# Performance work log

Measured on AMD Instinct MI355X. Metric: run time of the kernel, lower is better.

## Reference

```python
import jax, jax.numpy as jnp
import numpy as np

B, L, DX, H = 2, 2048, 1024, 16
DQ = DK = DV = DR = 64


def setup_inputs() -> dict:
    key0 = jax.random.key(0)
    ks = jax.random.split(key0, 14)
    def lin(kw, kb, din, dout):
        s = 1.0 / np.sqrt(din)
        w = jax.random.uniform(kw, (din, dout), jnp.float32, -s, s)
        b = jax.random.uniform(kb, (dout,), jnp.float32, -s, s)
        return w, b
    value = jax.random.normal(ks[0], (B, L, DX), jnp.float32)
    key_t = jax.random.normal(ks[1], (B, L, DX), jnp.float32)
    query = jax.random.normal(ks[2], (B, L, DX), jnp.float32)
    mask = jnp.tril(jnp.ones((L, L), jnp.int32))[None, None]  # [1,1,L,L] causal
    Wq_w, Wq_b = lin(ks[3], ks[4], DX, DQ * H)
    Wk_w, Wk_b = lin(ks[5], ks[6], DX, DK * H)
    Wv_w, Wv_b = lin(ks[7], ks[8], DX, DV * H)
    Wr_w, Wr_b = lin(ks[9], ks[10], DX, DR * H)
    wo_w, wo_b = lin(ks[11], ks[12], DV * H, DX)
    return dict(value=value, key=key_t, query=query, mask=mask,
                Wq_w=Wq_w, Wq_b=Wq_b, Wk_w=Wk_w, Wk_b=Wk_b,
                Wv_w=Wv_w, Wv_b=Wv_b, Wr_w=Wr_w, Wr_b=Wr_b,
                wo_w=wo_w, wo_b=wo_b)


def reference(value, key, query, mask, Wq_w, Wq_b, Wk_w, Wk_b, Wv_w, Wv_b,
              Wr_w, Wr_b, wo_w, wo_b):
    N, Lq, _ = query.shape
    q = (query @ Wq_w + Wq_b).reshape(N, Lq, H, DQ)   # nqhd
    k = (key @ Wk_w + Wk_b).reshape(N, -1, H, DK)     # nkhd
    v = (value @ Wv_w + Wv_b).reshape(N, -1, H, DV)   # nlhd
    r = (query @ Wr_w + Wr_b).reshape(N, Lq, H, DR)   # computed but unused (as in source)
    del r
    scores = jnp.einsum('nqhd,nkhd->nhqk', q, k)      # [N,H,L,L] materialized
    scores = jnp.where(mask == 0, jnp.float32(-1e20), scores)
    scale = jnp.float32(np.sqrt(DX))  # source divides by embedding_size**0.5
    attn = jax.nn.softmax(scores / scale, axis=3)
    out = jnp.einsum('nhql,nlhd->nqhd', attn, v).reshape(N, Lq, H * DV)
    return out @ wo_w + wo_b
```

## Files before the change

### kernel.cpp

```cpp
#include <hip/hip_runtime.h>
#include <hip/hip_bf16.h>
#include <type_traits>

typedef __hip_bfloat16 bf16;
typedef __attribute__((ext_vector_type(4))) float f32x4;
typedef __attribute__((ext_vector_type(8))) short s16x8;

#define DEVINL __device__ __forceinline__

#if defined(__has_builtin) && __has_builtin(__builtin_amdgcn_exp2f)
#define FEXP2(x) __builtin_amdgcn_exp2f(x)
#else
#define FEXP2(x) __exp2f(x)
#endif

DEVINL s16x8 load16B(const void* p) {
  s16x8 v;
  __builtin_memcpy(&v, __builtin_assume_aligned(p, 16), 16);
  return v;
}
DEVINL void store16B(void* p, s16x8 v) {
  __builtin_memcpy(__builtin_assume_aligned(p, 16), &v, 16);
}
DEVINL s16x8 cvt8(const float* p) {
  f32x4 a, b;
  __builtin_memcpy(&a, __builtin_assume_aligned(p, 16), 16);
  __builtin_memcpy(&b, __builtin_assume_aligned(p + 4, 16), 16);
  union { s16x8 v; bf16 h[8]; } u;
#pragma unroll
  for (int i = 0; i < 4; i++) {
    u.h[i] = __float2bfloat16(a[i]);
    u.h[4 + i] = __float2bfloat16(b[i]);
  }
  return u.v;
}
DEVINL void gload_lds16(const bf16* g, bf16* l) {
  __builtin_amdgcn_global_load_lds(
      (__attribute__((address_space(1))) void*)(void*)const_cast<bf16*>(g),
      (__attribute__((address_space(3))) void*)l, 16, 0, 0);
}

static constexpr int SEQ = 2048;
#define QSCALE 0.04508422002778011f

__global__ __launch_bounds__(256) void k_transpose(
    const float* __restrict__ Wq, const float* __restrict__ Wk,
    const float* __restrict__ Wv, const float* __restrict__ Wo,
    bf16* __restrict__ dst) {
  __shared__ float t[64][65];
  const float* src = blockIdx.z == 0 ? Wq : blockIdx.z == 1 ? Wk
                   : blockIdx.z == 2 ? Wv : Wo;
  bf16* out = dst + (size_t)blockIdx.z * 1024 * 1024;
  const int r0 = blockIdx.y * 64, c0 = blockIdx.x * 64;
#pragma unroll
  for (int i = 0; i < 16; i++) {
    int e = i * 256 + threadIdx.x;
    int r = e >> 6, c = e & 63;
    t[r][c] = src[(size_t)(r0 + r) * 1024 + c0 + c];
  }
  __syncthreads();
#pragma unroll
  for (int i = 0; i < 16; i++) {
    int e = i * 256 + threadIdx.x;
    int r = e >> 6, c = e & 63;
    out[(size_t)(c0 + r) * 1024 + r0 + c] = __float2bfloat16(t[c][r]);
  }
}

__global__ __launch_bounds__(256) void k_cvt3(
    const float* __restrict__ q, const float* __restrict__ k,
    const float* __restrict__ v, bf16* __restrict__ dstbase) {
  const float* src = blockIdx.z == 0 ? q : blockIdx.z == 1 ? k : v;
  bf16* dst = dstbase + (size_t)blockIdx.z * 4194304;
  size_t i = ((size_t)blockIdx.x * 256 + threadIdx.x) * 8;
  store16B(dst + i, cvt8(src + i));
}

template <typename XT, int MODE>
DEVINL void gemm_body(const XT* __restrict__ X, const bf16* __restrict__ WT,
                      const float* __restrict__ bias, void* __restrict__ dstv,
                      const float scale, const int m0, const int n0,
                      bf16* As, bf16* Bs) {
  const int tid = threadIdx.x;
  const int w = tid >> 6, lane = tid & 63, lg = lane >> 4, li = lane & 15;
  const int wm = w >> 1, wn = w & 1;

  f32x4 acc[4][4] = {};

  for (int kt = 0; kt < 32; ++kt) {
    const int k0 = kt * 32;
#pragma unroll
    for (int j = 0; j < 2; j++) {
      const int cb = (j * 4 + w) * 64;
      const int c = cb + lane;
      const int r = c >> 2, kk = (c & 3) * 8;
      gload_lds16(WT + (size_t)(n0 + r) * 1024 + k0 + kk, Bs + cb * 8);
      if constexpr (std::is_same_v<XT, bf16>)
        gload_lds16(X + (size_t)(m0 + r) * 1024 + k0 + kk, As + cb * 8);
    }
    if constexpr (std::is_same_v<XT, float>) {
#pragma unroll
      for (int j = 0; j < 2; j++) {
        const int c = j * 256 + tid;
        const int r = c >> 2, kk = (c & 3) * 8;
        s16x8 a = cvt8(X + (size_t)(m0 + r) * 1024 + k0 + kk);
        store16B((char*)As + c * 16, a);
      }
    }
    __syncthreads();
    s16x8 af[4], bfv[4];
#pragma unroll
    for (int i = 0; i < 4; i++)
      af[i] = load16B((char*)As + (wm * 64 + i * 16 + li) * 64 + lg * 16);
#pragma unroll
    for (int j = 0; j < 4; j++)
      bfv[j] = load16B((char*)Bs + (wn * 64 + j * 16 + li) * 64 + lg * 16);
#pragma unroll
    for (int i = 0; i < 4; i++)
#pragma unroll
      for (int j = 0; j < 4; j++) {
        if constexpr (MODE == 0)
          acc[i][j] = __builtin_amdgcn_mfma_f32_16x16x32_bf16(
              bfv[j], af[i], acc[i][j], 0, 0, 0);
        else
          acc[i][j] = __builtin_amdgcn_mfma_f32_16x16x32_bf16(
              af[i], bfv[j], acc[i][j], 0, 0, 0);
      }
    __syncthreads();
  }

  if constexpr (MODE == 1) {
    bf16* dst = (bf16*)dstv;
#pragma unroll
    for (int j = 0; j < 4; j++) {
      const int n = n0 + wn * 64 + j * 16 + li;
      const float bv = bias[n];
#pragma unroll
      for (int i = 0; i < 4; i++) {
        const int mrow = m0 + wm * 64 + i * 16 + lg * 4;
        f32x4 a = acc[i][j];
        size_t base =
            (((size_t)(mrow >> 11) * 16 + (n >> 6)) * 64 + (n & 63)) * SEQ +
            (mrow & 2047);
        bf16 tmp[4];
#pragma unroll
        for (int r = 0; r < 4; r++) tmp[r] = __float2bfloat16(a[r] + bv);
        __builtin_memcpy(__builtin_assume_aligned(dst + base, 8), tmp, 8);
      }
    }
  } else if constexpr (MODE == 2) {
    float* dst = (float*)dstv;
#pragma unroll
    for (int j = 0; j < 4; j++) {
      const int n = n0 + wn * 64 + j * 16 + li;
      const float bv = bias[n];
#pragma unroll
      for (int i = 0; i < 4; i++) {
        const int mrow = m0 + wm * 64 + i * 16 + lg * 4;
        f32x4 a = acc[i][j];
#pragma unroll
        for (int r = 0; r < 4; r++)
          dst[(size_t)(mrow + r) * 1024 + n] = a[r] + bv;
      }
    }
  } else {
    f32x4 bias4[4];
#pragma unroll
    for (int j = 0; j < 4; j++)
      __builtin_memcpy(&bias4[j], bias + n0 + wn * 64 + j * 16 + lg * 4, 16);
    bf16* dst = (bf16*)dstv;
#pragma unroll
    for (int i = 0; i < 4; i++) {
      const int m = m0 + wm * 64 + i * 16 + li;
      const int l = m & 2047, bb = m >> 11;
#pragma unroll
      for (int j = 0; j < 4; j++) {
        const int nb = n0 + wn * 64 + j * 16 + lg * 4;
        bf16 tmp[4];
#pragma unroll
        for (int r = 0; r < 4; r++)
          tmp[r] = __float2bfloat16((acc[i][j][r] + bias4[j][r]) * scale);
        size_t idx = (((size_t)bb * 16 + (nb >> 6)) * SEQ + l) * 64 + (nb & 63);
        __builtin_memcpy(__builtin_assume_aligned(dst + idx, 8), tmp, 8);
      }
    }
  }
}

__global__ __launch_bounds__(256) void k_gemm_qkv_bf16(
    const bf16* __restrict__ xbase, const bf16* __restrict__ WTbase,
    const float* __restrict__ qb, const float* __restrict__ kb,
    const float* __restrict__ vb, bf16* __restrict__ qo,
    bf16* __restrict__ ko, bf16* __restrict__ vto) {
  __shared__ alignas(16) bf16 As[128 * 32];
  __shared__ alignas(16) bf16 Bs[128 * 32];
  const int z = blockIdx.z;
  const bf16* X = xbase + (size_t)z * 4194304;
  const bf16* WT = WTbase + (size_t)z * 1048576;
  const float* bias = z == 0 ? qb : z == 1 ? kb : vb;
  if (z == 2)
    gemm_body<bf16, 1>(X, WT, bias, (void*)vto, 1.0f, blockIdx.x * 128,
                       blockIdx.y * 128, As, Bs);
  else
    gemm_body<bf16, 0>(X, WT, bias, z == 0 ? (void*)qo : (void*)ko,
                       z == 0 ? QSCALE : 1.0f, blockIdx.x * 128,
                       blockIdx.y * 128, As, Bs);
}

__global__ __launch_bounds__(256) void k_gemm_qkv_f32(
    const float* __restrict__ qx, const float* __restrict__ kx,
    const float* __restrict__ vx, const bf16* __restrict__ WTbase,
    const float* __restrict__ qb, const float* __restrict__ kb,
    const float* __restrict__ vb, bf16* __restrict__ qo,
    bf16* __restrict__ ko, bf16* __restrict__ vto) {
  __shared__ alignas(16) bf16 As[128 * 32];
  __shared__ alignas(16) bf16 Bs[128 * 32];
  const int z = blockIdx.z;
  const float* X = z == 0 ? qx : z == 1 ? kx : vx;
  const bf16* WT = WTbase + (size_t)z * 1048576;
  const float* bias = z == 0 ? qb : z == 1 ? kb : vb;
  if (z == 2)
    gemm_body<float, 1>(X, WT, bias, (void*)vto, 1.0f, blockIdx.x * 128,
                        blockIdx.y * 128, As, Bs);
  else
    gemm_body<float, 0>(X, WT, bias, z == 0 ? (void*)qo : (void*)ko,
                        z == 0 ? QSCALE : 1.0f, blockIdx.x * 128,
                        blockIdx.y * 128, As, Bs);
}

__global__ __launch_bounds__(256) void k_gemm_out(
    const bf16* __restrict__ X, const bf16* __restrict__ WT,
    const float* __restrict__ bias, float* __restrict__ out) {
  __shared__ alignas(16) bf16 As[128 * 32];
  __shared__ alignas(16) bf16 Bs[128 * 32];
  gemm_body<bf16, 2>(X, WT, bias, (void*)out, 1.0f, blockIdx.x * 128,
                     blockIdx.y * 128, As, Bs);
}

__global__ __launch_bounds__(256) void k_attn(
    const bf16* __restrict__ qb, const bf16* __restrict__ kb,
    const bf16* __restrict__ vtb, bf16* __restrict__ attn) {
  __shared__ alignas(16) bf16 Ks[2][64 * 64];
  __shared__ alignas(16) bf16 Vts[2][64 * 64];
  __shared__ alignas(16) bf16 Ps[4][16 * 64];
  const int tid = threadIdx.x;
  const int w = tid >> 6, lane = tid & 63, lg = lane >> 4, li = lane & 15;
  const int bh = blockIdx.x;
  const int y = blockIdx.y;
  const bf16* qh = qb + (size_t)bh * SEQ * 64;
  const bf16* kh = kb + (size_t)bh * SEQ * 64;
  const bf16* vth = vtb + (size_t)bh * 64 * SEQ;

  const int c0s = tid, c1s = 256 + tid;
  const int by0 = (c0s * 16) ^ (((c0s >> 3) & 7) << 4);
  const int by1 = (c1s * 16) ^ (((c1s >> 3) & 7) << 4);
  const int d0 = c0s >> 3, kk0 = (c0s & 7) * 8;
  const int d1 = c1s >> 3, kk1 = (c1s & 7) * 8;
  const int psw = (li & 7) << 3;
  const int b = bh >> 4, h = bh & 15;
  const int sb = (lane & 48);

#pragma unroll
  for (int half = 0; half < 2; half++) {
    const int qblk = half == 0 ? 31 - y : y;
    const int qrow = qblk * 64 + w * 16;

    s16x8 aq[2];
#pragma unroll
    for (int c = 0; c < 2; c++)
      aq[c] = load16B(qh + (size_t)(qrow + li) * 64 + c * 32 + lg * 8);

    f32x4 o[4] = {};
    float m_run = -1e38f;
    float l_run = 0.f;

    s16x8 rk[2], rv[2];
    rk[0] = load16B(kh + (size_t)c0s * 8);
    rk[1] = load16B(kh + (size_t)c1s * 8);
    rv[0] = load16B(vth + (size_t)d0 * SEQ + kk0);
    rv[1] = load16B(vth + (size_t)d1 * SEQ + kk1);
    store16B((char*)Ks[0] + by0, rk[0]);
    store16B((char*)Ks[0] + by1, rk[1]);
    store16B((char*)Vts[0] + by0, rv[0]);
    store16B((char*)Vts[0] + by1, rv[1]);
    if (qblk >= 1) {
      rk[0] = load16B(kh + (size_t)64 * 64 + c0s * 8);
      rk[1] = load16B(kh + (size_t)64 * 64 + c1s * 8);
      rv[0] = load16B(vth + (size_t)d0 * SEQ + 64 + kk0);
      rv[1] = load16B(vth + (size_t)d1 * SEQ + 64 + kk1);
    }
    __syncthreads();

    for (int kbk = 0; kbk <= qblk; ++kbk) {
      const int cur = kbk & 1;
      if (kbk < qblk) {
        store16B((char*)Ks[cur ^ 1] + by0, rk[0]);
        store16B((char*)Ks[cur ^ 1] + by1, rk[1]);
        store16B((char*)Vts[cur ^ 1] + by0, rv[0]);
        store16B((char*)Vts[cur ^ 1] + by1, rv[1]);
        if (kbk + 2 <= qblk) {
          const int kn = (kbk + 2) * 64;
          rk[0] = load16B(kh + (size_t)kn * 64 + c0s * 8);
          rk[1] = load16B(kh + (size_t)kn * 64 + c1s * 8);
          rv[0] = load16B(vth + (size_t)d0 * SEQ + kn + kk0);
          rv[1] = load16B(vth + (size_t)d1 * SEQ + kn + kk1);
        }
      }

      f32x4 s[4];
      __builtin_amdgcn_s_setprio(1);
#pragma unroll
      for (int t = 0; t < 4; t++) {
        f32x4 z = {};
#pragma unroll
        for (int c = 0; c < 2; c++) {
          int row = t * 16 + li;
          s16x8 ak =
              load16B((char*)Ks[cur] +
                      ((row * 128 + c * 64 + lg * 16) ^ ((row & 7) << 4)));
          z = __builtin_amdgcn_mfma_f32_16x16x32_bf16(ak, aq[c], z, 0, 0, 0);
        }
        s[t] = z;
      }
      __builtin_amdgcn_s_setprio(0);

      if (kbk == qblk) {
        const int kb0 = kbk * 64 + lg * 4;
        const int qg = qrow + li;
#pragma unroll
        for (int t = 0; t < 4; t++)
#pragma unroll
          for (int r = 0; r < 4; r++)
            if (kb0 + t * 16 + r > qg) s[t][r] = -1e30f;
      }

      f32x4 mm = s[0];
#pragma unroll
      for (int t = 1; t < 4; t++)
#pragma unroll
        for (int r = 0; r < 4; r++) mm[r] = fmaxf(mm[r], s[t][r]);
      float mr = fmaxf(fmaxf(mm[0], mm[1]), fmaxf(mm[2], mm[3]));
      mr = fmaxf(mr, __shfl_xor(mr, 16));
      mr = fmaxf(mr, __shfl_xor(mr, 32));

      const bool grow = !__all(mr <= m_run + 8.0f);
      const float mn = grow ? fmaxf(m_run, mr) : m_run;

      float p[4][4];
      float s0 = 0.f, s1 = 0.f, s2 = 0.f, s3 = 0.f;
#pragma unroll
      for (int r = 0; r < 4; r++) {
        float p0 = FEXP2(s[0][r] - mn), p1 = FEXP2(s[1][r] - mn);
        float p2 = FEXP2(s[2][r] - mn), p3 = FEXP2(s[3][r] - mn);
        p[0][r] = p0; p[1][r] = p1; p[2][r] = p2; p[3][r] = p3;
        s0 += p0; s1 += p1; s2 += p2; s3 += p3;
      }
      float sum = (s0 + s1) + (s2 + s3);
      sum += __shfl_xor(sum, 16);
      sum += __shfl_xor(sum, 32);

      if (grow) {
        const float cr = FEXP2(m_run - mn);
        l_run = l_run * cr + sum;
        m_run = mn;
        float crr[4];
#pragma unroll
        for (int r = 0; r < 4; r++) crr[r] = __shfl(cr, sb + (sb >> 2) + r);
#pragma unroll
        for (int t = 0; t < 4; t++)
#pragma unroll
          for (int r = 0; r < 4; r++) o[t][r] *= crr[r];
      } else {
        l_run += sum;
      }

#pragma unroll
      for (int t = 0; t < 4; t++) {
        bf16 tmp[4];
#pragma unroll
        for (int r = 0; r < 4; r++) tmp[r] = __float2bfloat16(p[t][r]);
        __builtin_memcpy(
            __builtin_assume_aligned(
                &Ps[w][li * 64 + ((t * 16 + lg * 4) ^ psw)], 8),
            tmp, 8);
      }

      s16x8 ap[2];
#pragma unroll
      for (int c = 0; c < 2; c++)
        ap[c] = load16B(&Ps[w][li * 64 + ((c * 32 + lg * 8) ^ psw)]);

      __builtin_amdgcn_s_setprio(1);
#pragma unroll
      for (int t = 0; t < 4; t++) {
#pragma unroll
        for (int c = 0; c < 2; c++) {
          int row = t * 16 + li;
          s16x8 bv =
              load16B((char*)Vts[cur] +
                      ((row * 128 + c * 64 + lg * 16) ^ ((row & 7) << 4)));
          o[t] =
              __builtin_amdgcn_mfma_f32_16x16x32_bf16(ap[c], bv, o[t], 0, 0, 0);
        }
      }
      __builtin_amdgcn_s_setprio(0);
      __syncthreads();
    }

    const float inv = 1.0f / l_run;
    float invr[4];
#pragma unroll
    for (int r = 0; r < 4; r++) invr[r] = __shfl(inv, sb + (sb >> 2) + r);
#pragma unroll
    for (int r = 0; r < 4; r++)
#pragma unroll
      for (int t = 0; t < 4; t++) {
        size_t idx = (size_t)(b * SEQ + qrow + lg * 4 + r) * 1024 + h * 64 +
                     t * 16 + li;
        attn[idx] = __float2bfloat16(o[t][r] * invr[r]);
      }
  }
}

extern "C" void kernel_launch(void* const* d_in, const int* in_sizes, int n_in,
                              void* d_out, int out_size, void* d_ws,
                              size_t ws_size, hipStream_t stream) {
  (void)in_sizes; (void)n_in; (void)out_size;
  const float* value = (const float*)d_in[0];
  const float* key   = (const float*)d_in[1];
  const float* query = (const float*)d_in[2];
  const float* Wq_w = (const float*)d_in[4];
  const float* Wq_b = (const float*)d_in[5];
  const float* Wk_w = (const float*)d_in[6];
  const float* Wk_b = (const float*)d_in[7];
  const float* Wv_w = (const float*)d_in[8];
  const float* Wv_b = (const float*)d_in[9];
  const float* wo_w = (const float*)d_in[12];
  const float* wo_b = (const float*)d_in[13];

  bf16* ws = (bf16*)d_ws;
  const size_t MM = 1048576;
  bf16* WT = ws;

  k_transpose<<<dim3(16, 16, 4), 256, 0, stream>>>(Wq_w, Wk_w, Wv_w, wo_w, WT);

  if (ws_size >= 28ull * MM * 2) {
    bf16* xbuf = ws + 4 * MM;
    bf16* qbuf = ws + 16 * MM;
    bf16* kbuf = ws + 20 * MM;
    bf16* vtbf = ws + 24 * MM;
    bf16* abuf = ws + 4 * MM;
    k_cvt3<<<dim3(2048, 1, 3), 256, 0, stream>>>(query, key, value, xbuf);
    k_gemm_qkv_bf16<<<dim3(32, 8, 3), 256, 0, stream>>>(
        xbuf, WT, Wq_b, Wk_b, Wv_b, qbuf, kbuf, vtbf);
    k_attn<<<dim3(32, 16), 256, 0, stream>>>(qbuf, kbuf, vtbf, abuf);
    k_gemm_out<<<dim3(32, 8), 256, 0, stream>>>(abuf, WT + 3 * MM, wo_b,
                                                (float*)d_out);
  } else {
    bf16* qbuf = ws + 4 * MM;
    bf16* kbuf = ws + 8 * MM;
    bf16* vtbf = ws + 12 * MM;
    bf16* abuf = ws + 16 * MM;
    k_gemm_qkv_f32<<<dim3(32, 8, 3), 256, 0, stream>>>(
        query, key, value, WT, Wq_b, Wk_b, Wv_b, qbuf, kbuf, vtbf);
    k_attn<<<dim3(32, 16), 256, 0, stream>>>(qbuf, kbuf, vtbf, abuf);
    k_gemm_out<<<dim3(32, 8), 256, 0, stream>>>(abuf, WT + 3 * MM, wo_b,
                                                (float*)d_out);
  }
}
```

Before: 126.7 us.

## Split long causal attention query blocks over KV halves and merge partials

Each attention block now handles one query block instead of a paired long/short pair. The 16 longest query blocks per head are split into two KV-range halves, each writing unnormalized bf16 partial outputs plus running max and sum. A new combine kernel merges the halves with the log-sum-exp rescale. This is meant to balance work across more blocks (1536 instead of 512) and shorten the critical path, at the cost of an extra launch, partial-output traffic, and bf16 rounding of the partials.

```diff
diff --git a/kernel.cpp b/kernel.cpp
--- a/kernel.cpp
+++ b/kernel.cpp
@@ -237,9 +237,11 @@
                      blockIdx.y * 128, As, Bs);
 }
 
+template <bool SPLIT>
 __global__ __launch_bounds__(256) void k_attn(
     const bf16* __restrict__ qb, const bf16* __restrict__ kb,
-    const bf16* __restrict__ vtb, bf16* __restrict__ attn) {
+    const bf16* __restrict__ vtb, bf16* __restrict__ attn,
+    bf16* __restrict__ po_base, float* __restrict__ pml_base) {
   __shared__ alignas(16) bf16 Ks[2][64 * 64];
   __shared__ alignas(16) bf16 Vts[2][64 * 64];
   __shared__ alignas(16) bf16 Ps[4][16 * 64];
@@ -247,9 +249,35 @@
   const int w = tid >> 6, lane = tid & 63, lg = lane >> 4, li = lane & 15;
   const int bh = blockIdx.x;
   const int y = blockIdx.y;
+  int qblk, kstart, kend, pidx;
+  if constexpr (SPLIT) {
+    if (y < 32) {
+      qblk = 31 - (y >> 1);
+      const int part = y & 1;
+      const int half = (qblk + 1) >> 1;
+      kstart = part ? half : 0;
+      kend = part ? qblk : half - 1;
+      pidx = ((bh << 4) + (qblk - 16)) * 2 + part;
+    } else {
+      qblk = 47 - y; kstart = 0; kend = qblk; pidx = -1;
+    }
+  } else {
+    qblk = (y < 8) ? 31 - y : (y < 16) ? y + 8 : (y < 24) ? 31 - y : y - 24;
+    kstart = 0; kend = qblk; pidx = -1;
+  }
+  const int qrow = qblk * 64 + w * 16;
   const bf16* qh = qb + (size_t)bh * SEQ * 64;
   const bf16* kh = kb + (size_t)bh * SEQ * 64;
   const bf16* vth = vtb + (size_t)bh * 64 * SEQ;
+
+  s16x8 aq[2];
+#pragma unroll
+  for (int c = 0; c < 2; c++)
+    aq[c] = load16B(qh + (size_t)(qrow + li) * 64 + c * 32 + lg * 8);
+
+  f32x4 o[4] = {};
+  float m_run = -1e38f;
+  float l_run = 0.f;
 
   const int c0s = tid, c1s = 256 + tid;
   const int by0 = (c0s * 16) ^ (((c0s >> 3) & 7) << 4);
@@ -257,156 +285,161 @@
   const int d0 = c0s >> 3, kk0 = (c0s & 7) * 8;
   const int d1 = c1s >> 3, kk1 = (c1s & 7) * 8;
   const int psw = (li & 7) << 3;
-  const int b = bh >> 4, h = bh & 15;
   const int sb = (lane & 48);
 
-#pragma unroll
-  for (int half = 0; half < 2; half++) {
-    const int qblk = half == 0 ? 31 - y : y;
-    const int qrow = qblk * 64 + w * 16;
-
-    s16x8 aq[2];
-#pragma unroll
-    for (int c = 0; c < 2; c++)
-      aq[c] = load16B(qh + (size_t)(qrow + li) * 64 + c * 32 + lg * 8);
-
-    f32x4 o[4] = {};
-    float m_run = -1e38f;
-    float l_run = 0.f;
-
-    s16x8 rk[2], rv[2];
-    rk[0] = load16B(kh + (size_t)c0s * 8);
-    rk[1] = load16B(kh + (size_t)c1s * 8);
-    rv[0] = load16B(vth + (size_t)d0 * SEQ + kk0);
-    rv[1] = load16B(vth + (size_t)d1 * SEQ + kk1);
+  s16x8 rk[2], rv[2];
+  {
+    const int k0b = kstart * 64;
+    rk[0] = load16B(kh + (size_t)k0b * 64 + c0s * 8);
+    rk[1] = load16B(kh + (size_t)k0b * 64 + c1s * 8);
+    rv[0] = load16B(vth + (size_t)d0 * SEQ + k0b + kk0);
+    rv[1] = load16B(vth + (size_t)d1 * SEQ + k0b + kk1);
     store16B((char*)Ks[0] + by0, rk[0]);
     store16B((char*)Ks[0] + by1, rk[1]);
     store16B((char*)Vts[0] + by0, rv[0]);
     store16B((char*)Vts[0] + by1, rv[1]);
-    if (qblk >= 1) {
-      rk[0] = load16B(kh + (size_t)64 * 64 + c0s * 8);
-      rk[1] = load16B(kh + (size_t)64 * 64 + c1s * 8);
-      rv[0] = load16B(vth + (size_t)d0 * SEQ + 64 + kk0);
-      rv[1] = load16B(vth + (size_t)d1 * SEQ + 64 + kk1);
-    }
+    if (kstart + 1 <= kend) {
+      const int k1b = (kstart + 1) * 64;
+      rk[0] = load16B(kh + (size_t)k1b * 64 + c0s * 8);
+      rk[1] = load16B(kh + (size_t)k1b * 64 + c1s * 8);
+      rv[0] = load16B(vth + (size_t)d0 * SEQ + k1b + kk0);
+      rv[1] = load16B(vth + (size_t)d1 * SEQ + k1b + kk1);
+    }
+  }
+  __syncthreads();
+
+  for (int kbk = kstart; kbk <= kend; ++kbk) {
+    const int cur = (kbk - kstart) & 1;
+    if (kbk < kend) {
+      store16B((char*)Ks[cur ^ 1] + by0, rk[0]);
+      store16B((char*)Ks[cur ^ 1] + by1, rk[1]);
+      store16B((char*)Vts[cur ^ 1] + by0, rv[0]);
+      store16B((char*)Vts[cur ^ 1] + by1, rv[1]);
+      if (kbk + 2 <= kend) {
+        const int kn = (kbk + 2) * 64;
+        rk[0] = load16B(kh + (size_t)kn * 64 + c0s * 8);
+        rk[1] = load16B(kh + (size_t)kn * 64 + c1s * 8);
+        rv[0] = load16B(vth + (size_t)d0 * SEQ + kn + kk0);
+        rv[1] = load16B(vth + (size_t)d1 * SEQ + kn + kk1);
+      }
+    }
+
+    f32x4 s[4];
+    __builtin_amdgcn_s_setprio(1);
+#pragma unroll
+    for (int t = 0; t < 4; t++) {
+      f32x4 z = {};
+#pragma unroll
+      for (int c = 0; c < 2; c++) {
+        int row = t * 16 + li;
+        s16x8 ak = load16B((char*)Ks[cur] +
+                           ((row * 128 + c * 64 + lg * 16) ^ ((row & 7) << 4)));
+        z = __builtin_amdgcn_mfma_f32_16x16x32_bf16(ak, aq[c], z, 0, 0, 0);
+      }
+      s[t] = z;
+    }
+    __builtin_amdgcn_s_setprio(0);
+
+    if (kbk == qblk) {
+      const int kb0 = kbk * 64 + lg * 4;
+      const int qg = qrow + li;
+#pragma unroll
+      for (int t = 0; t < 4; t++)
+#pragma unroll
+        for (int r = 0; r < 4; r++)
+          if (kb0 + t * 16 + r > qg) s[t][r] = -1e30f;
+    }
+
+    f32x4 mm = s[0];
+#pragma unroll
+    for (int t = 1; t < 4; t++)
+#pragma unroll
+      for (int r = 0; r < 4; r++) mm[r] = fmaxf(mm[r], s[t][r]);
+    float mr = fmaxf(fmaxf(mm[0], mm[1]), fmaxf(mm[2], mm[3]));
+    mr = fmaxf(mr, __shfl_xor(mr, 16));
+    mr = fmaxf(mr, __shfl_xor(mr, 32));
+
+    const bool grow = !__all(mr <= m_run + 8.0f);
+    const float mn = grow ? fmaxf(m_run, mr) : m_run;
+
+    float p[4][4];
+    float s0 = 0.f, s1 = 0.f, s2 = 0.f, s3 = 0.f;
+#pragma unroll
+    for (int r = 0; r < 4; r++) {
+      float p0 = FEXP2(s[0][r] - mn), p1 = FEXP2(s[1][r] - mn);
+      float p2 = FEXP2(s[2][r] - mn), p3 = FEXP2(s[3][r] - mn);
+      p[0][r] = p0; p[1][r] = p1; p[2][r] = p2; p[3][r] = p3;
+      s0 += p0; s1 += p1; s2 += p2; s3 += p3;
+    }
+    float sum = (s0 + s1) + (s2 + s3);
+    sum += __shfl_xor(sum, 16);
+    sum += __shfl_xor(sum, 32);
+
+    if (grow) {
+      const float cr = FEXP2(m_run - mn);
+      l_run = l_run * cr + sum;
+      m_run = mn;
+      float crr[4];
+#pragma unroll
+      for (int r = 0; r < 4; r++) crr[r] = __shfl(cr, sb + (sb >> 2) + r);
+#pragma unroll
+      for (int t = 0; t < 4; t++)
+#pragma unroll
+        for (int r = 0; r < 4; r++) o[t][r] *= crr[r];
+    } else {
+      l_run += sum;
+    }
+
+#pragma unroll
+    for (int t = 0; t < 4; t++) {
+      bf16 tmp[4];
+#pragma unroll
+      for (int r = 0; r < 4; r++) tmp[r] = __float2bfloat16(p[t][r]);
+      __builtin_memcpy(
+          __builtin_assume_aligned(
+              &Ps[w][li * 64 + ((t * 16 + lg * 4) ^ psw)], 8),
+          tmp, 8);
+    }
+
+    s16x8 ap[2];
+#pragma unroll
+    for (int c = 0; c < 2; c++)
+      ap[c] = load16B(&Ps[w][li * 64 + ((c * 32 + lg * 8) ^ psw)]);
+
+    __builtin_amdgcn_s_setprio(1);
+#pragma unroll
+    for (int t = 0; t < 4; t++) {
+#pragma unroll
+      for (int c = 0; c < 2; c++) {
+        int row = t * 16 + li;
+        s16x8 bv = load16B((char*)Vts[cur] +
+                           ((row * 128 + c * 64 + lg * 16) ^ ((row & 7) << 4)));
+        o[t] = __builtin_amdgcn_mfma_f32_16x16x32_bf16(ap[c], bv, o[t], 0, 0, 0);
+      }
+    }
+    __builtin_amdgcn_s_setprio(0);
     __syncthreads();
-
-    for (int kbk = 0; kbk <= qblk; ++kbk) {
-      const int cur = kbk & 1;
-      if (kbk < qblk) {
-        store16B((char*)Ks[cur ^ 1] + by0, rk[0]);
-        store16B((char*)Ks[cur ^ 1] + by1, rk[1]);
-        store16B((char*)Vts[cur ^ 1] + by0, rv[0]);
-        store16B((char*)Vts[cur ^ 1] + by1, rv[1]);
-        if (kbk + 2 <= qblk) {
-          const int kn = (kbk + 2) * 64;
-          rk[0] = load16B(kh + (size_t)kn * 64 + c0s * 8);
-          rk[1] = load16B(kh + (size_t)kn * 64 + c1s * 8);
-          rv[0] = load16B(vth + (size_t)d0 * SEQ + kn + kk0);
-          rv[1] = load16B(vth + (size_t)d1 * SEQ + kn + kk1);
-        }
-      }
-
-      f32x4 s[4];
-      __builtin_amdgcn_s_setprio(1);
-#pragma unroll
-      for (int t = 0; t < 4; t++) {
-        f32x4 z = {};
-#pragma unroll
-        for (int c = 0; c < 2; c++) {
-          int row = t * 16 + li;
-          s16x8 ak =
-              load16B((char*)Ks[cur] +
-                      ((row * 128 + c * 64 + lg * 16) ^ ((row & 7) << 4)));
-          z = __builtin_amdgcn_mfma_f32_16x16x32_bf16(ak, aq[c], z, 0, 0, 0);
-        }
-        s[t] = z;
-      }
-      __builtin_amdgcn_s_setprio(0);
-
-      if (kbk == qblk) {
-        const int kb0 = kbk * 64 + lg * 4;
-        const int qg = qrow + li;
-#pragma unroll
-        for (int t = 0; t < 4; t++)
-#pragma unroll
-          for (int r = 0; r < 4; r++)
-            if (kb0 + t * 16 + r > qg) s[t][r] = -1e30f;
-      }
-
-      f32x4 mm = s[0];
-#pragma unroll
-      for (int t = 1; t < 4; t++)
-#pragma unroll
-        for (int r = 0; r < 4; r++) mm[r] = fmaxf(mm[r], s[t][r]);
-      float mr = fmaxf(fmaxf(mm[0], mm[1]), fmaxf(mm[2], mm[3]));
-      mr = fmaxf(mr, __shfl_xor(mr, 16));
-      mr = fmaxf(mr, __shfl_xor(mr, 32));
-
-      const bool grow = !__all(mr <= m_run + 8.0f);
-      const float mn = grow ? fmaxf(m_run, mr) : m_run;
-
-      float p[4][4];
-      float s0 = 0.f, s1 = 0.f, s2 = 0.f, s3 = 0.f;
-#pragma unroll
-      for (int r = 0; r < 4; r++) {
-        float p0 = FEXP2(s[0][r] - mn), p1 = FEXP2(s[1][r] - mn);
-        float p2 = FEXP2(s[2][r] - mn), p3 = FEXP2(s[3][r] - mn);
-        p[0][r] = p0; p[1][r] = p1; p[2][r] = p2; p[3][r] = p3;
-        s0 += p0; s1 += p1; s2 += p2; s3 += p3;
-      }
-      float sum = (s0 + s1) + (s2 + s3);
-      sum += __shfl_xor(sum, 16);
-      sum += __shfl_xor(sum, 32);
-
-      if (grow) {
-        const float cr = FEXP2(m_run - mn);
-        l_run = l_run * cr + sum;
-        m_run = mn;
-        float crr[4];
-#pragma unroll
-        for (int r = 0; r < 4; r++) crr[r] = __shfl(cr, sb + (sb >> 2) + r);
-#pragma unroll
-        for (int t = 0; t < 4; t++)
-#pragma unroll
-          for (int r = 0; r < 4; r++) o[t][r] *= crr[r];
-      } else {
-        l_run += sum;
-      }
-
-#pragma unroll
-      for (int t = 0; t < 4; t++) {
-        bf16 tmp[4];
-#pragma unroll
-        for (int r = 0; r < 4; r++) tmp[r] = __float2bfloat16(p[t][r]);
-        __builtin_memcpy(
-            __builtin_assume_aligned(
-                &Ps[w][li * 64 + ((t * 16 + lg * 4) ^ psw)], 8),
-            tmp, 8);
-      }
-
-      s16x8 ap[2];
-#pragma unroll
-      for (int c = 0; c < 2; c++)
-        ap[c] = load16B(&Ps[w][li * 64 + ((c * 32 + lg * 8) ^ psw)]);
-
-      __builtin_amdgcn_s_setprio(1);
-#pragma unroll
-      for (int t = 0; t < 4; t++) {
-#pragma unroll
-        for (int c = 0; c < 2; c++) {
-          int row = t * 16 + li;
-          s16x8 bv =
-              load16B((char*)Vts[cur] +
-                      ((row * 128 + c * 64 + lg * 16) ^ ((row & 7) << 4)));
-          o[t] =
-              __builtin_amdgcn_mfma_f32_16x16x32_bf16(ap[c], bv, o[t], 0, 0, 0);
-        }
-      }
-      __builtin_amdgcn_s_setprio(0);
-      __syncthreads();
-    }
-
+  }
+
+  if (SPLIT && pidx >= 0) {
+    bf16* po = po_base + (size_t)pidx * 4096;
+#pragma unroll
+    for (int t = 0; t < 4; t++) {
+      bf16 tmp[4];
+#pragma unroll
+      for (int r = 0; r < 4; r++) tmp[r] = __float2bfloat16(o[t][r]);
+      __builtin_memcpy(
+          __builtin_assume_aligned(po + (t * 16 + li) * 64 + w * 16 + lg * 4,
+                                   8),
+          tmp, 8);
+    }
+    if (lg == 0) {
+      float* ml = pml_base + (size_t)pidx * 128;
+      ml[w * 16 + li] = m_run;
+      ml[64 + w * 16 + li] = l_run;
+    }
+  } else {
+    const int b = bh >> 4, h = bh & 15;
     const float inv = 1.0f / l_run;
     float invr[4];
 #pragma unroll
@@ -419,6 +452,32 @@
                      t * 16 + li;
         attn[idx] = __float2bfloat16(o[t][r] * invr[r]);
       }
+  }
+}
+
+__global__ __launch_bounds__(256) void k_combine(
+    const bf16* __restrict__ po_base, const float* __restrict__ pml_base,
+    bf16* __restrict__ attn) {
+  const int u = blockIdx.x;
+  const int bh = u >> 4, qblk = 16 + (u & 15);
+  const int tid = threadIdx.x;
+  const int d = tid >> 2, r0 = (tid & 3) * 16;
+  const bf16* o0 = po_base + (size_t)(u * 2) * 4096 + d * 64 + r0;
+  const bf16* o1 = o0 + 4096;
+  const float* ml0 = pml_base + (size_t)(u * 2) * 128;
+  const float* ml1 = ml0 + 128;
+  const int b = bh >> 4, h = bh & 15;
+#pragma unroll
+  for (int i = 0; i < 16; i++) {
+    const int row = r0 + i;
+    const float ma = ml0[row], mb = ml1[row];
+    const float m = fmaxf(ma, mb);
+    const float c0 = FEXP2(ma - m), c1 = FEXP2(mb - m);
+    const float l = ml0[64 + row] * c0 + ml1[64 + row] * c1;
+    const float v = (__bfloat162float(o0[i]) * c0 +
+                     __bfloat162float(o1[i]) * c1) / l;
+    attn[(size_t)(b * SEQ + qblk * 64 + row) * 1024 + h * 64 + d] =
+        __float2bfloat16(v);
   }
 }
 
@@ -450,10 +509,14 @@
     bf16* kbuf = ws + 20 * MM;
     bf16* vtbf = ws + 24 * MM;
     bf16* abuf = ws + 4 * MM;
+    bf16* po   = ws + 8 * MM;
+    float* pml = (float*)(ws + 12 * MM);
     k_cvt3<<<dim3(2048, 1, 3), 256, 0, stream>>>(query, key, value, xbuf);
     k_gemm_qkv_bf16<<<dim3(32, 8, 3), 256, 0, stream>>>(
         xbuf, WT, Wq_b, Wk_b, Wv_b, qbuf, kbuf, vtbf);
-    k_attn<<<dim3(32, 16), 256, 0, stream>>>(qbuf, kbuf, vtbf, abuf);
+    k_attn<true><<<dim3(32, 48), 256, 0, stream>>>(qbuf, kbuf, vtbf, abuf,
+                                                   po, pml);
+    k_combine<<<dim3(512), 256, 0, stream>>>(po, pml, abuf);
     k_gemm_out<<<dim3(32, 8), 256, 0, stream>>>(abuf, WT + 3 * MM, wo_b,
                                                 (float*)d_out);
   } else {
@@ -463,7 +526,8 @@
     bf16* abuf = ws + 16 * MM;
     k_gemm_qkv_f32<<<dim3(32, 8, 3), 256, 0, stream>>>(
         query, key, value, WT, Wq_b, Wk_b, Wv_b, qbuf, kbuf, vtbf);
-    k_attn<<<dim3(32, 16), 256, 0, stream>>>(qbuf, kbuf, vtbf, abuf);
+    k_attn<false><<<dim3(32, 32), 256, 0, stream>>>(qbuf, kbuf, vtbf, abuf,
+                                                    nullptr, nullptr);
     k_gemm_out<<<dim3(32, 8), 256, 0, stream>>>(abuf, WT + 3 * MM, wo_b,
                                                 (float*)d_out);
   }
```

Measured after the change: 137.6 us. 1.09x slower.
